# Optimization experiments

Measured on AMD Instinct MI355X. Metric: run time of the kernel, lower is better.

## Reference

```python
import jax, jax.numpy as jnp
import numpy as np

B, T = 32768, 32
OBJ_V, PRED_V = 179, 46
E_OBJ, E_PRED, H = 5, 5, 32
IN_DIM = E_OBJ + E_PRED + 2 + 4  # 16, matches LSTMCell input size


def setup_inputs() -> dict:
    key = jax.random.key(0)
    ks = jax.random.split(key, 12)
    s = 0.1
    return {
        "input_objects": jax.random.randint(ks[0], (B, T), 0, OBJ_V),
        "input_boxes": jax.random.uniform(ks[1], (B, T, 4), dtype=jnp.float32),
        "predicates": jax.random.randint(ks[2], (B, T), 0, PRED_V),
        "subject_indicators": jax.random.randint(ks[3], (B, T), 0, 2),
        "target_object": jax.random.randint(ks[4], (B,), 0, OBJ_V),
        "obj_emb": jax.random.normal(ks[5], (OBJ_V, E_OBJ), dtype=jnp.float32) * s,
        "pred_emb": jax.random.normal(ks[6], (PRED_V, E_PRED), dtype=jnp.float32) * s,
        "W_ih": jax.random.normal(ks[7], (4 * H, IN_DIM), dtype=jnp.float32) * s,
        "W_hh": jax.random.normal(ks[8], (4 * H, H), dtype=jnp.float32) * s,
        "b_ih": jnp.zeros((4 * H,), dtype=jnp.float32),
        "b_hh": jnp.zeros((4 * H,), dtype=jnp.float32),
        "fc2_W": jax.random.normal(ks[9], (4, H), dtype=jnp.float32) * s,
        "fc2_b": jnp.zeros((4,), dtype=jnp.float32),
    }


def _forward(input_objects, input_boxes, predicates, subject_indicators,
             obj_emb, pred_emb, W_ih, W_hh, b_ih, b_hh, fc2_W, fc2_b):
    # concatenate_features, vectorized over all timesteps at once: [B,T,16]
    feats = jnp.concatenate([
        obj_emb[input_objects],                                   # [B,T,5]
        pred_emb[predicates],                                     # [B,T,5]
        jax.nn.one_hot(subject_indicators, 2, dtype=jnp.float32), # [B,T,2]
        input_boxes,                                              # [B,T,4]
    ], axis=-1)
    xs = jnp.transpose(feats, (1, 0, 2))  # [T,B,16] for scan over time

    def step(carry, x):
        h, c = carry
        gates = x @ W_ih.T + b_ih + h @ W_hh.T + b_hh  # [B,4H]
        i, f, g, o = jnp.split(gates, 4, axis=-1)      # torch gate order i,f,g,o
        i = jax.nn.sigmoid(i)
        f = jax.nn.sigmoid(f)
        g = jnp.tanh(g)
        o = jax.nn.sigmoid(o)
        c = f * c + i * g
        h = o * jnp.tanh(c)
        return (h, c), None

    h0 = jnp.zeros((input_objects.shape[0], H), dtype=jnp.float32)
    (h, _), _ = jax.lax.scan(step, (h0, h0), xs)
    out = h @ fc2_W.T + fc2_b          # output_fc2 on last hidden state
    return jnp.clip(out, 0.0, 1.0)     # torch.clamp(min=0, max=1)


def reference(input_objects, input_boxes, predicates, subject_indicators, target_object,
              obj_emb, pred_emb, W_ih, W_hh, b_ih, b_hh, fc2_W, fc2_b):
    # target_object is accepted by the torch forward but unused in its body
    return _forward(input_objects, input_boxes, predicates, subject_indicators,
                    obj_emb, pred_emb, W_ih, W_hh, b_ih, b_hh, fc2_W, fc2_b)
```

## Files before the change

### kernel.cpp

```cpp
#include <hip/hip_runtime.h>

#define LDS_BYTES 18720

typedef _Float16 f16x8 __attribute__((ext_vector_type(8)));
typedef float    f32x4 __attribute__((ext_vector_type(4)));

#define LOG2E     1.44269504088896f
#define TWO_LOG2E 2.88539008177793f

__device__ __forceinline__ float sig_pre(float a) {
    return __builtin_amdgcn_rcpf(1.0f + __builtin_amdgcn_exp2f(a));
}
__device__ __forceinline__ float tanh_pre(float a) {
    return 1.0f - 2.0f * __builtin_amdgcn_rcpf(1.0f + __builtin_amdgcn_exp2f(a));
}
__device__ __forceinline__ int pack2(float a, float b) {
    union { _Float16 h[2]; int i; } u;
    u.h[0] = (_Float16)a; u.h[1] = (_Float16)b;
    return u.i;
}

__global__ __launch_bounds__(256, 8)
void lstm_fused(const int* __restrict__ objs,
                const float* __restrict__ boxes,
                const int* __restrict__ preds,
                const int* __restrict__ subj,
                const float* __restrict__ obj_emb,
                const float* __restrict__ pred_emb,
                const float* __restrict__ W_ih,
                const float* __restrict__ W_hh,
                const float* __restrict__ b_ih,
                const float* __restrict__ b_hh,
                const float* __restrict__ fc2_W,
                const float* __restrict__ fc2_b,
                float* __restrict__ out)
{
    extern __shared__ char smem[];
    const int tid  = threadIdx.x;
    const int lane = tid & 63;
    const int wv   = tid >> 6;
    const int quad = lane >> 4;
    const int cidx = lane & 15;
    const int XOFF = 0, HX0 = 16640, HX1 = 17664, ZOFF = 18688;

    if (tid < 8) ((int*)(smem + ZOFF))[tid] = 0;

    {
        int b  = tid >> 4;
        int t0 = (tid & 15) << 1;
        long gb = (long)blockIdx.x * 16 + b;
        int2 ov = *(const int2*)(objs  + gb * 32 + t0);
        int2 pv = *(const int2*)(preds + gb * 32 + t0);
        int2 sv = *(const int2*)(subj  + gb * 32 + t0);
        int oarr[2] = {ov.x, ov.y};
        int parr[2] = {pv.x, pv.y};
        int sarr[2] = {sv.x, sv.y};
        #pragma unroll
        for (int tt = 0; tt < 2; ++tt) {
            int t = t0 + tt;
            const float* eo = obj_emb  + oarr[tt] * 5;
            const float* ep = pred_emb + parr[tt] * 5;
            float4 bx = *(const float4*)(boxes + (gb * 32 + t) * 4);
            f16x8 lo, hi;
            lo[0]=(_Float16)eo[0]; lo[1]=(_Float16)eo[1]; lo[2]=(_Float16)eo[2];
            lo[3]=(_Float16)eo[3]; lo[4]=(_Float16)eo[4];
            lo[5]=(_Float16)ep[0]; lo[6]=(_Float16)ep[1]; lo[7]=(_Float16)ep[2];
            hi[0]=(_Float16)ep[3]; hi[1]=(_Float16)ep[4];
            hi[2]=(_Float16)(sarr[tt]==0 ? 1.0f : 0.0f);
            hi[3]=(_Float16)(sarr[tt]==1 ? 1.0f : 0.0f);
            hi[4]=(_Float16)bx.x; hi[5]=(_Float16)bx.y;
            hi[6]=(_Float16)bx.z; hi[7]=(_Float16)bx.w;
            char* dst = smem + XOFF + b * 1040 + t * 32;
            *(f16x8*)dst        = lo;
            *(f16x8*)(dst + 16) = hi;
        }
    }

    f16x8 Wf[2][2];
    f32x4 bias4[2];
    #pragma unroll
    for (int tile = 0; tile < 2; ++tile) {
        int rm   = cidx & 3;
        int u    = 8 * (cidx >> 2) + 2 * wv + (rm & 1);
        int gate = tile * 2 + (rm >> 1);
        float scale = (gate == 2) ? TWO_LOG2E : -LOG2E;
        int n = gate * 32 + u;
        #pragma unroll
        for (int ks = 0; ks < 2; ++ks) {
            f16x8 v;
            #pragma unroll
            for (int jj = 0; jj < 8; ++jj) {
                int k = ks * 32 + quad * 8 + jj;
                float val = (k < 16) ? W_ih[n * 16 + k]
                          : (k >= 32) ? W_hh[n * 32 + (k - 32)]
                          : 0.0f;
                v[jj] = (_Float16)(val * scale);
            }
            Wf[tile][ks] = v;
        }
        #pragma unroll
        for (int r = 0; r < 4; ++r) {
            int ur = 8 * quad + 2 * wv + (r & 1);
            int gr = tile * 2 + (r >> 1);
            float sc = (gr == 2) ? TWO_LOG2E : -LOG2E;
            bias4[tile][r] = (b_ih[gr * 32 + ur] + b_hh[gr * 32 + ur]) * sc;
        }
    }

    const bool qlow = (quad < 2);
    int       xaddr = qlow ? (XOFF + cidx * 1040 + quad * 16) : ZOFF;
    const int xinc  = qlow ? 32 : 0;
    const int slot  = lane * 4;

    __syncthreads();

    f16x8 xfrag = *(const f16x8*)(smem + xaddr); xaddr += xinc;
    f32x4 accp[2];
    #pragma unroll
    for (int tile = 0; tile < 2; ++tile)
        accp[tile] = __builtin_amdgcn_mfma_f32_16x16x32_f16(Wf[tile][0], xfrag, bias4[tile], 0, 0, 0);

    union { int i[4]; f16x8 v; } hf;
    hf.i[0] = 0; hf.i[1] = 0; hf.i[2] = 0; hf.i[3] = 0;
    float cst[2] = {0, 0};
    float h0, h1;

    #pragma unroll 2
    for (int t = 0; t < 32; ++t) {
        f32x4 acc0 = __builtin_amdgcn_mfma_f32_16x16x32_f16(Wf[0][1], hf.v, accp[0], 0, 0, 0);
        f32x4 acc1 = __builtin_amdgcn_mfma_f32_16x16x32_f16(Wf[1][1], hf.v, accp[1], 0, 0, 0);

        f16x8 xn = *(const f16x8*)(smem + xaddr); xaddr += xinc;

        float i0 = sig_pre(acc0[0]);
        float i1 = sig_pre(acc0[1]);
        float f0 = sig_pre(acc0[2]);
        float f1 = sig_pre(acc0[3]);
        float g0 = tanh_pre(acc1[0]);
        float g1 = tanh_pre(acc1[1]);
        float o0 = sig_pre(acc1[2]);
        float o1 = sig_pre(acc1[3]);
        float c0 = fmaf(f0, cst[0], i0 * g0);
        float c1 = fmaf(f1, cst[1], i1 * g1);
        cst[0] = c0; cst[1] = c1;
        h0 = o0 * tanh_pre(c0 * TWO_LOG2E);
        h1 = o1 * tanh_pre(c1 * TWO_LOG2E);
        int pk = pack2(h0, h1);

        char* buf = smem + ((t & 1) ? HX1 : HX0);
        *(int*)(buf + wv * 256 + slot) = pk;

        accp[0] = __builtin_amdgcn_mfma_f32_16x16x32_f16(Wf[0][0], xn, bias4[0], 0, 0, 0);
        accp[1] = __builtin_amdgcn_mfma_f32_16x16x32_f16(Wf[1][0], xn, bias4[1], 0, 0, 0);

        __syncthreads();
        hf.i[0] = *(const int*)(buf + 0   + slot);
        hf.i[1] = *(const int*)(buf + 256 + slot);
        hf.i[2] = *(const int*)(buf + 512 + slot);
        hf.i[3] = *(const int*)(buf + 768 + slot);
    }

    __syncthreads();
    {
        int u0 = 8 * quad + 2 * wv;
        *(float2*)(smem + cidx * 144 + u0 * 4) = (float2){h0, h1};
    }
    __syncthreads();

    if (tid < 64) {
        int b = tid >> 2, jj = tid & 3;
        const float* fw   = fc2_W + jj * 32;
        const float* hrow = (const float*)(smem + b * 144);
        float s = fc2_b[jj];
        #pragma unroll
        for (int k = 0; k < 8; ++k) {
            float4 hv = *(const float4*)(hrow + k * 4);
            s += fw[k*4+0] * hv.x + fw[k*4+1] * hv.y
               + fw[k*4+2] * hv.z + fw[k*4+3] * hv.w;
        }
        s = fminf(fmaxf(s, 0.0f), 1.0f);
        out[(long)blockIdx.x * 64 + tid] = s;
    }
}

extern "C" void kernel_launch(void* const* d_in, const int* in_sizes, int n_in,
                              void* d_out, int out_size, void* d_ws, size_t ws_size,
                              hipStream_t stream)
{
    lstm_fused<<<2048, 256, LDS_BYTES, stream>>>(
        (const int*)d_in[0], (const float*)d_in[1], (const int*)d_in[2],
        (const int*)d_in[3],
        (const float*)d_in[5], (const float*)d_in[6],
        (const float*)d_in[7], (const float*)d_in[8],
        (const float*)d_in[9], (const float*)d_in[10],
        (const float*)d_in[11], (const float*)d_in[12],
        (float*)d_out);
}
```

Measured before the change: 138.3 us.

## Merge LSTM gate reciprocals, pack f32x2 math, stagger block starts, move barrier

Rewrites the gate nonlinearities algebraically so the cell update needs one reciprocal per element instead of four, and the hidden output needs one more, all in paired f32x2 form with a packed round-toward-zero f16 conversion. It also adds a per-block s_sleep stagger before the main loop to desynchronize blocks, and moves the barrier ahead of the next input MFMAs. The goal is to cut transcendental (rcp) count on the serial critical path and smooth contention between blocks. The risks are a larger overflow or precision range in the merged denominators (products of exponentials can reach inf) and idle time from the sleep stagger.

```diff
diff --git a/kernel.cpp b/kernel.cpp
--- a/kernel.cpp
+++ b/kernel.cpp
@@ -3,22 +3,12 @@
 #define LDS_BYTES 18720
 
 typedef _Float16 f16x8 __attribute__((ext_vector_type(8)));
+typedef __fp16   fp16x2 __attribute__((ext_vector_type(2)));
 typedef float    f32x4 __attribute__((ext_vector_type(4)));
+typedef float    f32x2 __attribute__((ext_vector_type(2)));
 
 #define LOG2E     1.44269504088896f
 #define TWO_LOG2E 2.88539008177793f
-
-__device__ __forceinline__ float sig_pre(float a) {
-    return __builtin_amdgcn_rcpf(1.0f + __builtin_amdgcn_exp2f(a));
-}
-__device__ __forceinline__ float tanh_pre(float a) {
-    return 1.0f - 2.0f * __builtin_amdgcn_rcpf(1.0f + __builtin_amdgcn_exp2f(a));
-}
-__device__ __forceinline__ int pack2(float a, float b) {
-    union { _Float16 h[2]; int i; } u;
-    u.h[0] = (_Float16)a; u.h[1] = (_Float16)b;
-    return u.i;
-}
 
 __global__ __launch_bounds__(256, 8)
 void lstm_fused(const int* __restrict__ objs,
@@ -112,6 +102,11 @@
     const int xinc  = qlow ? 32 : 0;
     const int slot  = lane * 4;
 
+    {
+        int del = (blockIdx.x * 37) & 31;
+        while (del--) asm volatile("s_sleep 2" ::: "memory");
+    }
+
     __syncthreads();
 
     f16x8 xfrag = *(const f16x8*)(smem + xaddr); xaddr += xinc;
@@ -122,8 +117,9 @@
 
     union { int i[4]; f16x8 v; } hf;
     hf.i[0] = 0; hf.i[1] = 0; hf.i[2] = 0; hf.i[3] = 0;
-    float cst[2] = {0, 0};
-    float h0, h1;
+    const f32x2 one = {1.0f, 1.0f};
+    f32x2 cstv = {0.0f, 0.0f};
+    f32x2 hv = {0.0f, 0.0f};
 
     #pragma unroll 2
     for (int t = 0; t < 32; ++t) {
@@ -132,28 +128,37 @@
 
         f16x8 xn = *(const f16x8*)(smem + xaddr); xaddr += xinc;
 
-        float i0 = sig_pre(acc0[0]);
-        float i1 = sig_pre(acc0[1]);
-        float f0 = sig_pre(acc0[2]);
-        float f1 = sig_pre(acc0[3]);
-        float g0 = tanh_pre(acc1[0]);
-        float g1 = tanh_pre(acc1[1]);
-        float o0 = sig_pre(acc1[2]);
-        float o1 = sig_pre(acc1[3]);
-        float c0 = fmaf(f0, cst[0], i0 * g0);
-        float c1 = fmaf(f1, cst[1], i1 * g1);
-        cst[0] = c0; cst[1] = c1;
-        h0 = o0 * tanh_pre(c0 * TWO_LOG2E);
-        h1 = o1 * tanh_pre(c1 * TWO_LOG2E);
-        int pk = pack2(h0, h1);
+        f32x2 Ei = {__builtin_amdgcn_exp2f(acc0[0]), __builtin_amdgcn_exp2f(acc0[1])};
+        f32x2 Ef = {__builtin_amdgcn_exp2f(acc0[2]), __builtin_amdgcn_exp2f(acc0[3])};
+        f32x2 Eg = {__builtin_amdgcn_exp2f(acc1[0]), __builtin_amdgcn_exp2f(acc1[1])};
+        f32x2 Eo = {__builtin_amdgcn_exp2f(acc1[2]), __builtin_amdgcn_exp2f(acc1[3])};
+
+        f32x2 t1  = Ei + one;
+        f32x2 dig = t1 * Eg + t1;
+        f32x2 tf  = Ef + one;
+        f32x2 nn  = (Eg - one) * tf + cstv * dig;
+        f32x2 den = tf * dig;
+        f32x2 rde = {__builtin_amdgcn_rcpf(den.x), __builtin_amdgcn_rcpf(den.y)};
+        f32x2 c   = nn * rde;
+        cstv = c;
+        f32x2 cl  = c * TWO_LOG2E;
+        f32x2 Ec  = {__builtin_amdgcn_exp2f(cl.x), __builtin_amdgcn_exp2f(cl.y)};
+        f32x2 to  = Eo + one;
+        f32x2 dh  = to * Ec + to;
+        f32x2 rdh = {__builtin_amdgcn_rcpf(dh.x), __builtin_amdgcn_rcpf(dh.y)};
+        hv = (Ec - one) * rdh;
+
+        union { fp16x2 h; int i; } pku;
+        pku.h = __builtin_amdgcn_cvt_pkrtz(hv.x, hv.y);
+        int pk = pku.i;
 
         char* buf = smem + ((t & 1) ? HX1 : HX0);
         *(int*)(buf + wv * 256 + slot) = pk;
+        __syncthreads();
 
         accp[0] = __builtin_amdgcn_mfma_f32_16x16x32_f16(Wf[0][0], xn, bias4[0], 0, 0, 0);
         accp[1] = __builtin_amdgcn_mfma_f32_16x16x32_f16(Wf[1][0], xn, bias4[1], 0, 0, 0);
 
-        __syncthreads();
         hf.i[0] = *(const int*)(buf + 0   + slot);
         hf.i[1] = *(const int*)(buf + 256 + slot);
         hf.i[2] = *(const int*)(buf + 512 + slot);
@@ -163,7 +168,7 @@
     __syncthreads();
     {
         int u0 = 8 * quad + 2 * wv;
-        *(float2*)(smem + cidx * 144 + u0 * 4) = (float2){h0, h1};
+        *(float2*)(smem + cidx * 144 + u0 * 4) = (float2){hv.x, hv.y};
     }
     __syncthreads();
 
@@ -174,9 +179,9 @@
         float s = fc2_b[jj];
         #pragma unroll
         for (int k = 0; k < 8; ++k) {
-            float4 hv = *(const float4*)(hrow + k * 4);
-            s += fw[k*4+0] * hv.x + fw[k*4+1] * hv.y
-               + fw[k*4+2] * hv.z + fw[k*4+3] * hv.w;
+            float4 hvv = *(const float4*)(hrow + k * 4);
+            s += fw[k*4+0] * hvv.x + fw[k*4+1] * hvv.y
+               + fw[k*4+2] * hvv.z + fw[k*4+3] * hvv.w;
         }
         s = fminf(fmaxf(s, 0.0f), 1.0f);
         out[(long)blockIdx.x * 64 + tid] = s;
```

Result: faster. 132.0 us (-4.5%).
